# Kernel optimization log

Hardware: AMD Instinct MI355X
Metric: run time of the kernel (lower is better)

Reference implementation:

```python
import jax, jax.numpy as jnp
import numpy as np

B, T, D = 2, 2048, 2048
H, KVH = 32, 8
HD = D // H            # 64
G = H // KVH           # 4


def setup_inputs() -> dict:
    key = jax.random.key(0)
    k1, k2, k3 = jax.random.split(key, 3)
    x_q = jax.random.normal(k1, (B, T, D), dtype=jnp.float32)
    W_qkv = jax.random.normal(k2, (D, H * HD + 2 * KVH * HD), dtype=jnp.float32) * 0.02
    W_out = jax.random.normal(k3, (D, D), dtype=jnp.float32) * 0.02
    b_out = jnp.zeros((D,), dtype=jnp.float32)
    # real rotary tables: theta = 10000^{-2i/HD}
    inv_freq = 1.0 / (10000.0 ** (np.arange(0, HD, 2) / HD))   # [HD/2]
    pos = np.arange(T)[:, None] * inv_freq[None, :]            # [T, HD/2]
    rope_cos = jnp.asarray(np.cos(pos), dtype=jnp.float32)
    rope_sin = jnp.asarray(np.sin(pos), dtype=jnp.float32)
    return {"x_q": x_q, "W_qkv": W_qkv, "W_out": W_out, "b_out": b_out,
            "rope_cos": rope_cos, "rope_sin": rope_sin}


def _apply_rope(x, cos, sin):
    # x: [B, h, T, HD], cos/sin: [T, HD/2] -> interleaved even/odd rotation
    xe = x[..., 0::2]
    xo = x[..., 1::2]
    c = cos[None, None, :, :]
    s = sin[None, None, :, :]
    return jnp.stack([xe * c - xo * s, xe * s + xo * c], axis=-1).reshape(x.shape)


def reference(x_q, W_qkv, W_out, b_out, rope_cos, rope_sin):
    b, t, d = x_q.shape
    qkv = x_q @ W_qkv                                  # [B,T,3072]
    q_lin = qkv[..., : H * HD]
    k_lin = qkv[..., H * HD: H * HD + KVH * HD]
    v_lin = qkv[..., H * HD + KVH * HD:]
    q = q_lin.reshape(b, t, H, HD).transpose(0, 2, 1, 3)        # [B,H,T,HD]
    k = k_lin.reshape(b, t, KVH, HD).transpose(0, 2, 1, 3)      # [B,KVH,T,HD]
    v = v_lin.reshape(b, t, KVH, HD).transpose(0, 2, 1, 3)
    # GQA expand (repeat_interleave over heads)
    k = jnp.repeat(k, G, axis=1)                                # [B,H,T,HD]
    v = jnp.repeat(v, G, axis=1)
    q = _apply_rope(q, rope_cos[:t], rope_sin[:t])
    k = _apply_rope(k, rope_cos[:t], rope_sin[:t])
    scale = 1.0 / jnp.sqrt(jnp.asarray(HD, dtype=x_q.dtype))
    logits = jnp.einsum('bhqd,bhkd->bhqk', q, k) * scale        # [B,H,T,T]
    causal = jnp.triu(jnp.ones((t, t), dtype=bool), 1)[None, None]
    logits = jnp.where(causal, jnp.finfo(logits.dtype).min, logits)
    attn = jax.nn.softmax(logits, axis=-1)
    out = jnp.einsum('bhqk,bhkd->bhqd', attn, v)                # [B,H,T,HD]
    out = out.transpose(0, 2, 1, 3).reshape(b, t, H * HD)       # [B,T,D]
    out = out @ W_out + b_out
    return jnp.nan_to_num(out, nan=0.0, posinf=1e4, neginf=-1e4)
```

## Files before the change

### kernel.cpp

```cpp
#include <hip/hip_runtime.h>
#include <hip/hip_bf16.h>

#define DI __device__ __forceinline__

#if __has_builtin(__builtin_amdgcn_exp2f)
#define EXP2(x) __builtin_amdgcn_exp2f(x)
#else
#define EXP2(x) exp2f(x)
#endif

namespace {

constexpr int Bc = 2, Tc = 2048, Dc = 2048, Hc = 32, KVHc = 8, HDc = 64;
constexpr int NQKV = Hc * HDc + 2 * KVHc * HDc;

typedef __bf16 bf16x8 __attribute__((ext_vector_type(8)));
typedef unsigned short u16x8 __attribute__((ext_vector_type(8)));
typedef unsigned short u16x4 __attribute__((ext_vector_type(4)));
typedef float f32x4 __attribute__((ext_vector_type(4)));

union FragU { u16x8 u; bf16x8 b; u16x4 h[2]; };

DI float bits2f(unsigned int u) {
  union { unsigned int i; float f; } v; v.i = u << 16; return v.f;
}
DI unsigned short f2bits(float f) {
  __hip_bfloat16 h = __float2bfloat16(f);
  return *reinterpret_cast<unsigned short*>(&h);
}

DI void store_out(float* p, float v) { *p = v; }
DI void store_out(__hip_bfloat16* p, float v) { *p = __float2bfloat16(v); }

typedef __attribute__((address_space(1))) void gv_t;
typedef __attribute__((address_space(3))) void lv_t;

template<int ROWB, int TOTB, bool SWZ = false>
DI void stage_tile(const char* g, long long row_stride_b, char* lds) {
  const int tid = threadIdx.x;
  const int wid = tid >> 6, lane = tid & 63;
#pragma unroll
  for (int it = 0; it < TOTB / 4096; ++it) {
    int off = it * 4096 + wid * 1024 + lane * 16;
    int row = off / ROWB;
    int colb = off % ROWB;
    if (SWZ) colb ^= (row & 7) << 4;
    const char* gp = g + (long long)row * row_stride_b + colb;
    char* lp = lds + it * 4096 + wid * 1024;
    __builtin_amdgcn_global_load_lds((gv_t*)gp, (lv_t*)lp, 16, 0, 0);
  }
}

__global__ __launch_bounds__(256) void cvt_f32_bf16(
    const float* __restrict__ in, __hip_bfloat16* __restrict__ out) {
  const long long i = ((long long)blockIdx.x * 256 + threadIdx.x) * 8;
  const float4 a = *(const float4*)(in + i);
  const float4 b = *(const float4*)(in + i + 4);
  u16x8 r;
  r[0] = f2bits(a.x); r[1] = f2bits(a.y); r[2] = f2bits(a.z); r[3] = f2bits(a.w);
  r[4] = f2bits(b.x); r[5] = f2bits(b.y); r[6] = f2bits(b.z); r[7] = f2bits(b.w);
  *(u16x8*)((unsigned short*)out + i) = r;
}

__global__ __launch_bounds__(256) void transpose_cvt_kernel(
    const float* __restrict__ in, __hip_bfloat16* __restrict__ out, int R, int C) {
  __shared__ unsigned short tile[64][65];
  const int c0 = blockIdx.x * 64, r0 = blockIdx.y * 64;
  const int tid = threadIdx.x;
  const int rr = tid >> 2, seg = (tid & 3) * 16;
  const float* src = in + (long long)(r0 + rr) * C + c0 + seg;
#pragma unroll
  for (int i = 0; i < 16; ++i) tile[rr][seg + i] = f2bits(src[i]);
  __syncthreads();
  unsigned short* dst = (unsigned short*)out + (long long)(c0 + rr) * R + r0 + seg;
#pragma unroll
  for (int i = 0; i < 16; ++i) dst[i] = tile[seg + i][rr];
}

__global__ __launch_bounds__(256) void transpose_kernel(
    const __hip_bfloat16* __restrict__ in, __hip_bfloat16* __restrict__ out,
    int R, int C) {
  __shared__ unsigned short tile[64][65];
  const long long slice = (long long)R * C;
  const unsigned short* ip = (const unsigned short*)in + (long long)blockIdx.z * slice;
  unsigned short* op = (unsigned short*)out + (long long)blockIdx.z * slice;
  const int c0 = blockIdx.x * 64, r0 = blockIdx.y * 64;
  const int tid = threadIdx.x;
  const int rr = tid >> 2, seg = (tid & 3) * 16;
  const unsigned short* src = ip + (long long)(r0 + rr) * C + c0 + seg;
#pragma unroll
  for (int i = 0; i < 16; ++i) tile[rr][seg + i] = src[i];
  __syncthreads();
  unsigned short* dst = op + (long long)(c0 + rr) * R + r0 + seg;
#pragma unroll
  for (int i = 0; i < 16; ++i) dst[i] = tile[seg + i][rr];
}

template <typename OT>
__global__ __launch_bounds__(256) void gemm_bt(
    const __hip_bfloat16* __restrict__ A, const __hip_bfloat16* __restrict__ Bt,
    const float* __restrict__ bias, OT* __restrict__ C, int M, int N, int K) {
  __shared__ __align__(16) char As[8192];
  __shared__ __align__(16) char Bs[8192];
  const int n0 = blockIdx.x * 128;
  const int m0 = blockIdx.y * 128;
  const int tid = threadIdx.x;
  const int wid = tid >> 6, lane = tid & 63;
  const int wm = (wid >> 1) * 64, wn = (wid & 1) * 64;
  const int l15 = lane & 15, quad = lane >> 4;

  f32x4 acc[4][4] = {};

  const int nk = K >> 5;
  for (int kt = 0; kt < nk; ++kt) {
    __syncthreads();
    stage_tile<64, 8192>((const char*)(A + (long long)m0 * K + kt * 32), (long long)K * 2, As);
    stage_tile<64, 8192>((const char*)(Bt + (long long)n0 * K + kt * 32), (long long)K * 2, Bs);
    __syncthreads();

    FragU a[4], b[4];
#pragma unroll
    for (int mt = 0; mt < 4; ++mt)
      a[mt].u = *(const u16x8*)(As + ((wm + mt * 16 + l15) * 32 + quad * 8) * 2);
#pragma unroll
    for (int nt = 0; nt < 4; ++nt)
      b[nt].u = *(const u16x8*)(Bs + ((wn + nt * 16 + l15) * 32 + quad * 8) * 2);
#pragma unroll
    for (int mt = 0; mt < 4; ++mt)
#pragma unroll
      for (int nt = 0; nt < 4; ++nt)
        acc[mt][nt] = __builtin_amdgcn_mfma_f32_16x16x32_bf16(a[mt].b, b[nt].b, acc[mt][nt], 0, 0, 0);
  }

#pragma unroll
  for (int nt = 0; nt < 4; ++nt) {
    const int col = n0 + wn + nt * 16 + l15;
    const float bv = bias ? bias[col] : 0.f;
#pragma unroll
    for (int mt = 0; mt < 4; ++mt) {
#pragma unroll
      for (int r = 0; r < 4; ++r) {
        const int row = m0 + wm + mt * 16 + quad * 4 + r;
        store_out(C + (long long)row * N + col, acc[mt][nt][r] + bv);
      }
    }
  }
}

__global__ __launch_bounds__(384) void rope_reshape(
    const __hip_bfloat16* __restrict__ qkv, const float* __restrict__ cosb,
    const float* __restrict__ sinb, __hip_bfloat16* __restrict__ Qo,
    __hip_bfloat16* __restrict__ Ko, __hip_bfloat16* __restrict__ Vo) {
  constexpr float SCL = 0.125f * 1.44269504088896f;
  const int row = blockIdx.x;
  const int b = row / Tc, t = row % Tc;
  const unsigned short* src = (const unsigned short*)qkv + (long long)row * NQKV;
  const float* cb = cosb + t * 32;
  const float* sb = sinb + t * 32;
  const int e = (int)threadIdx.x * 8;
  const u16x8 v = *(const u16x8*)(src + e);
  if (e < Hc * HDc) {
    const int hh = e >> 6, d = e & 63, ii = d >> 1;
    u16x8 r;
#pragma unroll
    for (int p = 0; p < 4; ++p) {
      const float c = cb[ii + p], s = sb[ii + p];
      const float xe = bits2f(v[2 * p]), xo = bits2f(v[2 * p + 1]);
      r[2 * p] = f2bits((xe * c - xo * s) * SCL);
      r[2 * p + 1] = f2bits((xe * s + xo * c) * SCL);
    }
    const long long idx = (((long long)b * Hc + hh) * Tc + t) * HDc + d;
    *(u16x8*)((unsigned short*)Qo + idx) = r;
  } else if (e < Hc * HDc + KVHc * HDc) {
    const int e2 = e - Hc * HDc;
    const int kh = e2 >> 6, d = e2 & 63, ii = d >> 1;
    u16x8 r;
#pragma unroll
    for (int p = 0; p < 4; ++p) {
      const float c = cb[ii + p], s = sb[ii + p];
      const float xe = bits2f(v[2 * p]), xo = bits2f(v[2 * p + 1]);
      r[2 * p] = f2bits(xe * c - xo * s);
      r[2 * p + 1] = f2bits(xe * s + xo * c);
    }
    const long long idx = (((long long)b * KVHc + kh) * Tc + t) * HDc + d;
    *(u16x8*)((unsigned short*)Ko + idx) = r;
  } else {
    const int e2 = e - (Hc * HDc + KVHc * HDc);
    const int kh = e2 >> 6, d = e2 & 63;
    const long long idx = (((long long)b * KVHc + kh) * Tc + t) * HDc + d;
    *(u16x8*)((unsigned short*)Vo + idx) = v;
  }
}

DI void attn_tile(const char* __restrict__ Ksb, const char* __restrict__ Vsb,
                  const FragU (&qa)[2], f32x4 (&O)[4], float& m_i, float& l_i,
                  bool diag, int wid, int l15, int quad, int sw) {
  f32x4 S[4] = {};
#pragma unroll
  for (int nt = 0; nt < 4; ++nt) {
#pragma unroll
    for (int ks = 0; ks < 2; ++ks) {
      FragU kb;
      kb.u = *(const u16x8*)(Ksb + (nt * 16 + l15) * 128 + ((((ks << 2) | quad) ^ sw) << 4));
      S[nt] = __builtin_amdgcn_mfma_f32_16x16x32_bf16(kb.b, qa[ks].b, S[nt], 0, 0, 0);
    }
  }

  if (diag) {
#pragma unroll
    for (int nt = 0; nt < 4; ++nt)
#pragma unroll
      for (int r = 0; r < 4; ++r)
        if ((nt * 16 + quad * 4 + r) > (wid * 16 + l15)) S[nt][r] = -1e30f;
  }

  float mx = fmaxf(fmaxf(S[0][0], S[0][1]), fmaxf(S[0][2], S[0][3]));
#pragma unroll
  for (int nt = 1; nt < 4; ++nt)
    mx = fmaxf(mx, fmaxf(fmaxf(S[nt][0], S[nt][1]), fmaxf(S[nt][2], S[nt][3])));
  mx = fmaxf(mx, __shfl_xor(mx, 16, 64));
  mx = fmaxf(mx, __shfl_xor(mx, 32, 64));
  const float mnew = fmaxf(m_i, mx);
  const float alpha = EXP2(m_i - mnew);
  m_i = mnew;

  float pe[4][4];
  float sum = 0.f;
#pragma unroll
  for (int nt = 0; nt < 4; ++nt)
#pragma unroll
    for (int r = 0; r < 4; ++r) {
      const float p = EXP2(S[nt][r] - mnew);
      pe[nt][r] = p;
      sum += p;
    }
  sum += __shfl_xor(sum, 16, 64);
  sum += __shfl_xor(sum, 32, 64);
  l_i = l_i * alpha + sum;

  FragU pa[2];
#pragma unroll
  for (int ks = 0; ks < 2; ++ks)
#pragma unroll
    for (int r = 0; r < 4; ++r) {
      pa[ks].u[r] = f2bits(pe[2 * ks][r]);
      pa[ks].u[4 + r] = f2bits(pe[2 * ks + 1][r]);
    }
#pragma unroll
  for (int nt = 0; nt < 4; ++nt)
#pragma unroll
    for (int r = 0; r < 4; ++r) O[nt][r] *= alpha;

#pragma unroll
  for (int nt = 0; nt < 4; ++nt) {
    const char* vrow = Vsb + (nt * 16 + l15) * 128 + ((quad & 1) << 3);
    const int gq = quad >> 1;
#pragma unroll
    for (int ks = 0; ks < 2; ++ks) {
      FragU vb;
      vb.h[0] = *(const u16x4*)(vrow + (((ks * 4 + gq) ^ sw) << 4));
      vb.h[1] = *(const u16x4*)(vrow + (((ks * 4 + gq + 2) ^ sw) << 4));
      O[nt] = __builtin_amdgcn_mfma_f32_16x16x32_bf16(vb.b, pa[ks].b, O[nt], 0, 0, 0);
    }
  }
}

__global__ __launch_bounds__(256, 4) void attn_kernel(
    const __hip_bfloat16* __restrict__ Q, const __hip_bfloat16* __restrict__ K,
    const __hip_bfloat16* __restrict__ Vt, __hip_bfloat16* __restrict__ Out) {
  __shared__ __align__(16) char Ks[2][8192];
  __shared__ __align__(16) char Vs[2][8192];

  const int p = blockIdx.x;
  const int qtA = p, qtB = (Tc / 64 - 1) - p;
  const int h = blockIdx.y, b = blockIdx.z;
  const int kvh = h >> 2;
  const int tid = threadIdx.x, wid = tid >> 6, lane = tid & 63;
  const int l15 = lane & 15, quad = lane >> 4;
  const int sw = l15 & 7;

  const char* QgA = (const char*)(Q + (((long long)b * Hc + h) * Tc + qtA * 64) * HDc);
  const char* QgB = (const char*)(Q + (((long long)b * Hc + h) * Tc + qtB * 64) * HDc);
  const char* Kg = (const char*)(K + (((long long)b * KVHc + kvh) * Tc) * HDc);
  const char* Vg = (const char*)(Vt + (((long long)b * KVHc + kvh) * HDc) * Tc);

  FragU qaA[2], qaB[2];
#pragma unroll
  for (int ks = 0; ks < 2; ++ks) {
    const int qoff = (wid * 16 + l15) * 128 + (((ks << 2) | quad) << 4);
    qaA[ks].u = *(const u16x8*)(QgA + qoff);
    qaB[ks].u = *(const u16x8*)(QgB + qoff);
  }

  f32x4 OA[4] = {}, OB[4] = {};
  float mA = -1e30f, lA = 0.f, mB = -1e30f, lB = 0.f;

  stage_tile<128, 8192, true>(Kg, 128, Ks[0]);
  stage_tile<128, 8192, true>(Vg, (long long)Tc * 2, Vs[0]);
  asm volatile("s_waitcnt vmcnt(0)" ::: "memory");
  __syncthreads();

  for (int j = 0; j <= qtB; ++j) {
    const int cur = j & 1;
    if (j < qtB) {
      stage_tile<128, 8192, true>(Kg + (long long)(j + 1) * 8192, 128, Ks[cur ^ 1]);
      stage_tile<128, 8192, true>(Vg + (long long)(j + 1) * 128, (long long)Tc * 2, Vs[cur ^ 1]);
    }

    attn_tile(Ks[cur], Vs[cur], qaB, OB, mB, lB, j == qtB, wid, l15, quad, sw);
    if (j <= qtA)
      attn_tile(Ks[cur], Vs[cur], qaA, OA, mA, lA, j == qtA, wid, l15, quad, sw);

    asm volatile("s_waitcnt vmcnt(0)" ::: "memory");
    __syncthreads();
  }

  const float invA = 1.0f / lA, invB = 1.0f / lB;
  const int tA = qtA * 64 + wid * 16 + l15;
  const int tB = qtB * 64 + wid * 16 + l15;
  unsigned short* obA =
      (unsigned short*)Out + ((long long)b * Tc + tA) * Dc + h * 64 + quad * 4;
  unsigned short* obB =
      (unsigned short*)Out + ((long long)b * Tc + tB) * Dc + h * 64 + quad * 4;
#pragma unroll
  for (int nt = 0; nt < 4; ++nt) {
    u16x4 va, vb;
#pragma unroll
    for (int r = 0; r < 4; ++r) {
      va[r] = f2bits(OA[nt][r] * invA);
      vb[r] = f2bits(OB[nt][r] * invB);
    }
    *(u16x4*)(obA + nt * 16) = va;
    *(u16x4*)(obB + nt * 16) = vb;
  }
}

}

extern "C" void kernel_launch(void* const* d_in, const int* in_sizes, int n_in,
                              void* d_out, int out_size, void* d_ws, size_t ws_size,
                              hipStream_t stream) {
  const float* x_q  = (const float*)d_in[0];
  const float* Wqkv = (const float*)d_in[1];
  const float* Wout = (const float*)d_in[2];
  const float* bout = (const float*)d_in[3];
  const float* rc   = (const float*)d_in[4];
  const float* rs   = (const float*)d_in[5];
  float* out = (float*)d_out;

  constexpr size_t SZ_QKV   = (size_t)Bc * Tc * NQKV * 2;
  constexpr size_t SZ_XB    = (size_t)Bc * Tc * Dc * 2;
  constexpr size_t SZ_QB    = (size_t)Bc * Hc * Tc * HDc * 2;
  constexpr size_t SZ_KV    = (size_t)Bc * KVHc * Tc * HDc * 2;
  constexpr size_t SZ_AO    = (size_t)Bc * Tc * Dc * 2;
  constexpr size_t OFF_QKV   = 0;
  constexpr size_t OFF_XB    = SZ_QKV;
  constexpr size_t OFF_WQKVT = SZ_QKV + SZ_XB;
  constexpr size_t OFF_QB    = SZ_QKV;
  constexpr size_t OFF_KB    = OFF_QB + SZ_QB;
  constexpr size_t OFF_VTMP  = OFF_KB + SZ_KV;
  constexpr size_t OFF_VT    = 0;
  constexpr size_t OFF_AO    = SZ_KV;
  constexpr size_t OFF_WOUTT = OFF_AO + SZ_AO;

  char* w = (char*)d_ws;
  __hip_bfloat16* qkv   = (__hip_bfloat16*)(w + OFF_QKV);
  __hip_bfloat16* xb    = (__hip_bfloat16*)(w + OFF_XB);
  __hip_bfloat16* WqkvT = (__hip_bfloat16*)(w + OFF_WQKVT);
  __hip_bfloat16* Qb    = (__hip_bfloat16*)(w + OFF_QB);
  __hip_bfloat16* Kb    = (__hip_bfloat16*)(w + OFF_KB);
  __hip_bfloat16* Vtmp  = (__hip_bfloat16*)(w + OFF_VTMP);
  __hip_bfloat16* Vt    = (__hip_bfloat16*)(w + OFF_VT);
  __hip_bfloat16* AO    = (__hip_bfloat16*)(w + OFF_AO);
  __hip_bfloat16* WoutT = (__hip_bfloat16*)(w + OFF_WOUTT);

  cvt_f32_bf16<<<dim3((Bc * Tc * Dc) / (256 * 8)), 256, 0, stream>>>(x_q, xb);

  transpose_cvt_kernel<<<dim3(NQKV / 64, Dc / 64), 256, 0, stream>>>(Wqkv, WqkvT, Dc, NQKV);

  gemm_bt<__hip_bfloat16><<<dim3(NQKV / 128, (Bc * Tc) / 128), 256, 0, stream>>>(
      xb, WqkvT, nullptr, qkv, Bc * Tc, NQKV, Dc);

  rope_reshape<<<dim3(Bc * Tc), 384, 0, stream>>>(qkv, rc, rs, Qb, Kb, Vtmp);

  transpose_kernel<<<dim3(HDc / 64, Tc / 64, Bc * KVHc), 256, 0, stream>>>(Vtmp, Vt, Tc, HDc);

  attn_kernel<<<dim3(Tc / 128, Hc, Bc), 256, 0, stream>>>(Qb, Kb, Vt, AO);

  transpose_cvt_kernel<<<dim3(Dc / 64, Dc / 64), 256, 0, stream>>>(Wout, WoutT, Dc, Dc);

  gemm_bt<float><<<dim3(Dc / 128, (Bc * Tc) / 128), 256, 0, stream>>>(
      AO, WoutT, bout, out, Bc * Tc, Dc, Dc);
}
```

Baseline: 375.7 us.

## Process both query tiles per KV tile jointly with interleaved MFMAs and setprio

While both query tiles are active, a new dual-tile routine loads each K and V fragment from LDS once and feeds it to the MFMAs of both tiles. This halves the LDS reads in that phase and interleaves two independent MFMA chains, so the latency of one chain overlaps with the other. The MFMA sections are also wrapped in s_setprio raises so the wave keeps issuing once it reaches matrix work. The cost is more live accumulators and score registers, which under launch_bounds(256,4) could cause spills or lower occupancy.

```diff
diff --git a/kernel.cpp b/kernel.cpp
--- a/kernel.cpp
+++ b/kernel.cpp
@@ -192,28 +192,16 @@
   }
 }
 
-DI void attn_tile(const char* __restrict__ Ksb, const char* __restrict__ Vsb,
-                  const FragU (&qa)[2], f32x4 (&O)[4], float& m_i, float& l_i,
-                  bool diag, int wid, int l15, int quad, int sw) {
-  f32x4 S[4] = {};
-#pragma unroll
-  for (int nt = 0; nt < 4; ++nt) {
-#pragma unroll
-    for (int ks = 0; ks < 2; ++ks) {
-      FragU kb;
-      kb.u = *(const u16x8*)(Ksb + (nt * 16 + l15) * 128 + ((((ks << 2) | quad) ^ sw) << 4));
-      S[nt] = __builtin_amdgcn_mfma_f32_16x16x32_bf16(kb.b, qa[ks].b, S[nt], 0, 0, 0);
-    }
-  }
-
-  if (diag) {
-#pragma unroll
-    for (int nt = 0; nt < 4; ++nt)
-#pragma unroll
-      for (int r = 0; r < 4; ++r)
-        if ((nt * 16 + quad * 4 + r) > (wid * 16 + l15)) S[nt][r] = -1e30f;
-  }
-
+
+DI void mask_diag(f32x4 (&S)[4], int wid, int l15, int quad) {
+#pragma unroll
+  for (int nt = 0; nt < 4; ++nt)
+#pragma unroll
+    for (int r = 0; r < 4; ++r)
+      if ((nt * 16 + quad * 4 + r) > (wid * 16 + l15)) S[nt][r] = -1e30f;
+}
+
+DI float softmax_pack(f32x4 (&S)[4], float& m_i, float& l_i, FragU (&pa)[2]) {
   float mx = fmaxf(fmaxf(S[0][0], S[0][1]), fmaxf(S[0][2], S[0][3]));
 #pragma unroll
   for (int nt = 1; nt < 4; ++nt)
@@ -223,34 +211,51 @@
   const float mnew = fmaxf(m_i, mx);
   const float alpha = EXP2(m_i - mnew);
   m_i = mnew;
-
-  float pe[4][4];
   float sum = 0.f;
 #pragma unroll
   for (int nt = 0; nt < 4; ++nt)
 #pragma unroll
     for (int r = 0; r < 4; ++r) {
-      const float p = EXP2(S[nt][r] - mnew);
-      pe[nt][r] = p;
-      sum += p;
+      const float pp = EXP2(S[nt][r] - mnew);
+      S[nt][r] = pp;
+      sum += pp;
     }
   sum += __shfl_xor(sum, 16, 64);
   sum += __shfl_xor(sum, 32, 64);
   l_i = l_i * alpha + sum;
-
+#pragma unroll
+  for (int ks = 0; ks < 2; ++ks)
+#pragma unroll
+    for (int r = 0; r < 4; ++r) {
+      pa[ks].u[r] = f2bits(S[2 * ks][r]);
+      pa[ks].u[4 + r] = f2bits(S[2 * ks + 1][r]);
+    }
+  return alpha;
+}
+
+DI void attn_tile(const char* __restrict__ Ksb, const char* __restrict__ Vsb,
+                  const FragU (&qa)[2], f32x4 (&O)[4], float& m_i, float& l_i,
+                  bool diag, int wid, int l15, int quad, int sw) {
+  f32x4 S[4] = {};
+  __builtin_amdgcn_s_setprio(1);
+#pragma unroll
+  for (int nt = 0; nt < 4; ++nt) {
+#pragma unroll
+    for (int ks = 0; ks < 2; ++ks) {
+      FragU kb;
+      kb.u = *(const u16x8*)(Ksb + (nt * 16 + l15) * 128 + ((((ks << 2) | quad) ^ sw) << 4));
+      S[nt] = __builtin_amdgcn_mfma_f32_16x16x32_bf16(kb.b, qa[ks].b, S[nt], 0, 0, 0);
+    }
+  }
+  __builtin_amdgcn_s_setprio(0);
+  if (diag) mask_diag(S, wid, l15, quad);
   FragU pa[2];
-#pragma unroll
-  for (int ks = 0; ks < 2; ++ks)
-#pragma unroll
-    for (int r = 0; r < 4; ++r) {
-      pa[ks].u[r] = f2bits(pe[2 * ks][r]);
-      pa[ks].u[4 + r] = f2bits(pe[2 * ks + 1][r]);
-    }
+  const float alpha = softmax_pack(S, m_i, l_i, pa);
 #pragma unroll
   for (int nt = 0; nt < 4; ++nt)
 #pragma unroll
     for (int r = 0; r < 4; ++r) O[nt][r] *= alpha;
-
+  __builtin_amdgcn_s_setprio(1);
 #pragma unroll
   for (int nt = 0; nt < 4; ++nt) {
     const char* vrow = Vsb + (nt * 16 + l15) * 128 + ((quad & 1) << 3);
@@ -263,6 +268,53 @@
       O[nt] = __builtin_amdgcn_mfma_f32_16x16x32_bf16(vb.b, pa[ks].b, O[nt], 0, 0, 0);
     }
   }
+  __builtin_amdgcn_s_setprio(0);
+}
+
+DI void attn_tile_dual(const char* __restrict__ Ksb, const char* __restrict__ Vsb,
+                       const FragU (&qaB)[2], const FragU (&qaA)[2],
+                       f32x4 (&OB)[4], f32x4 (&OA)[4],
+                       float& mB, float& lB, float& mA, float& lA,
+                       bool diagA, int wid, int l15, int quad, int sw) {
+  f32x4 SB[4] = {}, SA[4] = {};
+  __builtin_amdgcn_s_setprio(1);
+#pragma unroll
+  for (int nt = 0; nt < 4; ++nt) {
+#pragma unroll
+    for (int ks = 0; ks < 2; ++ks) {
+      FragU kb;
+      kb.u = *(const u16x8*)(Ksb + (nt * 16 + l15) * 128 + ((((ks << 2) | quad) ^ sw) << 4));
+      SB[nt] = __builtin_amdgcn_mfma_f32_16x16x32_bf16(kb.b, qaB[ks].b, SB[nt], 0, 0, 0);
+      SA[nt] = __builtin_amdgcn_mfma_f32_16x16x32_bf16(kb.b, qaA[ks].b, SA[nt], 0, 0, 0);
+    }
+  }
+  __builtin_amdgcn_s_setprio(0);
+  if (diagA) mask_diag(SA, wid, l15, quad);
+  FragU paB[2], paA[2];
+  const float aB = softmax_pack(SB, mB, lB, paB);
+  const float aA = softmax_pack(SA, mA, lA, paA);
+#pragma unroll
+  for (int nt = 0; nt < 4; ++nt)
+#pragma unroll
+    for (int r = 0; r < 4; ++r) {
+      OB[nt][r] *= aB;
+      OA[nt][r] *= aA;
+    }
+  __builtin_amdgcn_s_setprio(1);
+#pragma unroll
+  for (int nt = 0; nt < 4; ++nt) {
+    const char* vrow = Vsb + (nt * 16 + l15) * 128 + ((quad & 1) << 3);
+    const int gq = quad >> 1;
+#pragma unroll
+    for (int ks = 0; ks < 2; ++ks) {
+      FragU vb;
+      vb.h[0] = *(const u16x4*)(vrow + (((ks * 4 + gq) ^ sw) << 4));
+      vb.h[1] = *(const u16x4*)(vrow + (((ks * 4 + gq + 2) ^ sw) << 4));
+      OB[nt] = __builtin_amdgcn_mfma_f32_16x16x32_bf16(vb.b, paB[ks].b, OB[nt], 0, 0, 0);
+      OA[nt] = __builtin_amdgcn_mfma_f32_16x16x32_bf16(vb.b, paA[ks].b, OA[nt], 0, 0, 0);
+    }
+  }
+  __builtin_amdgcn_s_setprio(0);
 }
 
 __global__ __launch_bounds__(256, 4) void attn_kernel(
@@ -307,9 +359,12 @@
       stage_tile<128, 8192, true>(Vg + (long long)(j + 1) * 128, (long long)Tc * 2, Vs[cur ^ 1]);
     }
 
-    attn_tile(Ks[cur], Vs[cur], qaB, OB, mB, lB, j == qtB, wid, l15, quad, sw);
-    if (j <= qtA)
-      attn_tile(Ks[cur], Vs[cur], qaA, OA, mA, lA, j == qtA, wid, l15, quad, sw);
+    if (j <= qtA) {
+      attn_tile_dual(Ks[cur], Vs[cur], qaB, qaA, OB, OA, mB, lB, mA, lA,
+                     j == qtA, wid, l15, quad, sw);
+    } else {
+      attn_tile(Ks[cur], Vs[cur], qaB, OB, mB, lB, j == qtB, wid, l15, quad, sw);
+    }
 
     asm volatile("s_waitcnt vmcnt(0)" ::: "memory");
     __syncthreads();
```

Result: faster. 349.9 us (-6.9%).
